# Optimization experiments

Measured on AMD Instinct MI355X. Metric: run time of the kernel, lower is better.

Reference implementation:

```python
import jax, jax.numpy as jnp
import numpy as np

E = 100    # n_estimators
F = 10     # max_features
D = 100    # input feature dim
N = 8192   # batch
LAT = 2    # latent_dim
ENC_DIMS = [F, F // 2, F // 4, LAT]          # 10 -> 5 -> 2 -> 2
DEC_DIMS = [LAT, D // 4, D // 2, D]          # 2 -> 25 -> 50 -> 100


def _make_mlp(key, dims):
    ws, bs = [], []
    for i, (din, dout) in enumerate(zip(dims[:-1], dims[1:])):
        k = jax.random.fold_in(key, i)
        ws.append(jax.random.normal(k, (E, din, dout), dtype=jnp.float32) * 0.05)
        bs.append(jnp.zeros((E, dout), dtype=jnp.float32))
    return ws, bs


def setup_inputs() -> dict:
    key = jax.random.key(0)
    k_in, k_idx, k_enc, k_hi, k_lo = jax.random.split(key, 5)
    inputs = jax.random.normal(k_in, (N, D), dtype=jnp.float32)
    # per-estimator random feature subsets (original uses choice w/o replacement)
    randsamples = jax.random.randint(k_idx, (E, F), 0, D, dtype=jnp.int32)
    enc_ws, enc_bs = _make_mlp(k_enc, ENC_DIMS)
    hi_ws, hi_bs = _make_mlp(k_hi, DEC_DIMS)
    lo_ws, lo_bs = _make_mlp(k_lo, DEC_DIMS)
    d = {"inputs": inputs, "randsamples": randsamples}
    for i in range(3):
        d[f"enc_w{i}"], d[f"enc_b{i}"] = enc_ws[i], enc_bs[i]
        d[f"hi_w{i}"], d[f"hi_b{i}"] = hi_ws[i], hi_bs[i]
        d[f"lo_w{i}"], d[f"lo_b{i}"] = lo_ws[i], lo_bs[i]
    return d


def _mlp(x, ws, bs):
    # x: [E, N, din]; linear activation throughout (module default)
    for w, b in zip(ws, bs):
        x = jnp.einsum('enf,efg->eng', x, w) + b[:, None, :]
    return x


def reference(inputs, randsamples,
              enc_w0, enc_b0, enc_w1, enc_b1, enc_w2, enc_b2,
              hi_w0, hi_b0, hi_w1, hi_b1, hi_w2, hi_b2,
              lo_w0, lo_b0, lo_w1, lo_b1, lo_w2, lo_b2):
    # batched feature gather: [N, E, F] -> [E, N, F]
    xg = jnp.transpose(jnp.take(inputs, randsamples, axis=1), (1, 0, 2))
    z = _mlp(xg, [enc_w0, enc_w1, enc_w2], [enc_b0, enc_b1, enc_b2])   # [E, N, LAT]
    o_hi = _mlp(z, [hi_w0, hi_w1, hi_w2], [hi_b0, hi_b1, hi_b2])       # [E, N, D]
    o_lo = _mlp(z, [lo_w0, lo_w1, lo_w2], [lo_b0, lo_b1, lo_b2])       # [E, N, D]
    return (o_hi, o_lo)
```

## Files before the change

kernel.cpp:

```cpp
#include <hip/hip_runtime.h>

#define E_  100
#define F_  10
#define D_  100
#define N_  8192
#define TN  256
#define NTILES (N_ / TN)

typedef float f32x4 __attribute__((ext_vector_type(4)));

#define OFF_WHI  0
#define OFF_BHI  200
#define OFF_WLO  300
#define OFF_BLO  500
#define OFF_WENC 600
#define OFF_BENC 620
#define WS_PER_E 624
#define OFF_T    (E_ * WS_PER_E)
#define WS_NEED_BYTES ((size_t)(OFF_T + D_ * N_) * 4)

template <bool DO_TRANSPOSE>
__global__ __launch_bounds__(128) void prep_kernel(
    const float* __restrict__ inputs,
    const float* __restrict__ enc_w0, const float* __restrict__ enc_b0,
    const float* __restrict__ enc_w1, const float* __restrict__ enc_b1,
    const float* __restrict__ enc_w2, const float* __restrict__ enc_b2,
    const float* __restrict__ hi_w0,  const float* __restrict__ hi_b0,
    const float* __restrict__ hi_w1,  const float* __restrict__ hi_b1,
    const float* __restrict__ hi_w2,  const float* __restrict__ hi_b2,
    const float* __restrict__ lo_w0,  const float* __restrict__ lo_b0,
    const float* __restrict__ lo_w1,  const float* __restrict__ lo_b1,
    const float* __restrict__ lo_w2,  const float* __restrict__ lo_b2,
    float* __restrict__ ws)
{
    const int t = threadIdx.x;

    if (DO_TRANSPOSE && blockIdx.x >= E_) {
        const int bi = blockIdx.x - E_;
        const int n0 = (bi >> 2) * 128;
        const int d0 = (bi & 3) * 25;
        float* T = ws + OFF_T;
        const float* rowp = inputs + (size_t)(n0 + t) * D_ + d0;
#pragma unroll 5
        for (int j = 0; j < 25; ++j)
            T[(size_t)(d0 + j) * N_ + n0 + t] = rowp[j];
        return;
    }

    const int e = blockIdx.x;
    float* wsE = ws + (size_t)e * WS_PER_E;

    {
        const float* w0 = enc_w0 + e * 50;
        const float* w1 = enc_w1 + e * 10;
        const float* w2 = enc_w2 + e * 4;
        const float* b0 = enc_b0 + e * 5;
        const float* b1 = enc_b1 + e * 2;
        const float* b2 = enc_b2 + e * 2;

        __shared__ float sW01[20];
        __shared__ float sB01[2];
        if (t < 20) {
            int f = t >> 1, g = t & 1;
            float s = 0.f;
            for (int k = 0; k < 5; ++k) s += w0[f * 5 + k] * w1[k * 2 + g];
            sW01[t] = s;
        }
        if (t < 2) {
            float s = b1[t];
            for (int k = 0; k < 5; ++k) s += b0[k] * w1[k * 2 + t];
            sB01[t] = s;
        }
        __syncthreads();
        if (t < 20) {
            int f = t >> 1, g2 = t & 1;
            wsE[OFF_WENC + t] = sW01[f * 2 + 0] * w2[0 * 2 + g2]
                              + sW01[f * 2 + 1] * w2[1 * 2 + g2];
        }
        if (t < 2) {
            wsE[OFF_BENC + t] = sB01[0] * w2[0 * 2 + t] + sB01[1] * w2[1 * 2 + t] + b2[t];
        }
        __syncthreads();
    }

    __shared__ float sT[100];
    __shared__ float sU[50];
    for (int dec = 0; dec < 2; ++dec) {
        const float* w0 = (dec ? lo_w0 : hi_w0) + e * 50;
        const float* w1 = (dec ? lo_w1 : hi_w1) + e * 1250;
        const float* w2 = (dec ? lo_w2 : hi_w2) + e * 5000;
        const float* b0 = (dec ? lo_b0 : hi_b0) + e * 25;
        const float* b1 = (dec ? lo_b1 : hi_b1) + e * 50;
        const float* b2 = (dec ? lo_b2 : hi_b2) + e * 100;
        float* W = wsE + (dec ? OFF_WLO : OFF_WHI);
        float* B = wsE + (dec ? OFF_BLO : OFF_BHI);

        for (int i = t; i < 100; i += blockDim.x) {
            int a = i / 50, c = i % 50;
            float s = 0.f;
            for (int b = 0; b < 25; ++b) s += w0[a * 25 + b] * w1[b * 50 + c];
            sT[i] = s;
        }
        for (int i = t; i < 50; i += blockDim.x) {
            float s = b1[i];
            for (int b = 0; b < 25; ++b) s += b0[b] * w1[b * 50 + i];
            sU[i] = s;
        }
        __syncthreads();
        for (int i = t; i < 200; i += blockDim.x) {
            int a = i / 100, d = i % 100;
            float s = 0.f;
            for (int c = 0; c < 50; ++c) s += sT[a * 50 + c] * w2[c * 100 + d];
            W[i] = s;
        }
        for (int i = t; i < 100; i += blockDim.x) {
            float s = b2[i];
            for (int c = 0; c < 50; ++c) s += sU[c] * w2[c * 100 + i];
            B[i] = s;
        }
        __syncthreads();
    }
}

template <bool USE_T>
__global__ __launch_bounds__(256) void rancoders_main(
    const float* __restrict__ inputs,
    const int*   __restrict__ randsamples,
    const float* __restrict__ ws,
    float* __restrict__ out)
{
    const int e    = blockIdx.x >> 5;
    const int tile = blockIdx.x & (NTILES - 1);
    const int n0   = tile * TN;
    const int t    = threadIdx.x;

    __shared__ __align__(16) float sP[WS_PER_E];
    __shared__ int    sIdx[F_];
    __shared__ float2 sZ2[TN];

    const float* wsE = ws + (size_t)e * WS_PER_E;
    for (int i = t; i < 622; i += 256) sP[i] = wsE[i];
    if (t < F_) sIdx[t] = randsamples[e * F_ + t];
    __syncthreads();

    {
        float z0 = sP[OFF_BENC + 0];
        float z1 = sP[OFF_BENC + 1];
        if (USE_T) {
            const float* T = ws + OFF_T;
#pragma unroll
            for (int f = 0; f < F_; ++f) {
                float v = T[(size_t)sIdx[f] * N_ + n0 + t];
                z0 += v * sP[OFF_WENC + 2 * f + 0];
                z1 += v * sP[OFF_WENC + 2 * f + 1];
            }
        } else {
            const float* row = inputs + (size_t)(n0 + t) * D_;
#pragma unroll
            for (int f = 0; f < F_; ++f) {
                float v = row[sIdx[f]];
                z0 += v * sP[OFF_WENC + 2 * f + 0];
                z1 += v * sP[OFF_WENC + 2 * f + 1];
            }
        }
        sZ2[t] = make_float2(z0, z1);
    }
    __syncthreads();

    const int w    = t >> 6;
    const int l    = t & 63;
    const int h    = l >> 5;
    const int dq   = l & 31;
    const bool act = (dq < 25);
    const int d    = (act ? dq : 24) * 4;

    const f32x4 w0h = *(const f32x4*)&sP[OFF_WHI + d];
    const f32x4 w1h = *(const f32x4*)&sP[OFF_WHI + 100 + d];
    const f32x4 bh  = *(const f32x4*)&sP[OFF_BHI + d];
    const f32x4 w0l = *(const f32x4*)&sP[OFF_WLO + d];
    const f32x4 w1l = *(const f32x4*)&sP[OFF_WLO + 100 + d];
    const f32x4 bl  = *(const f32x4*)&sP[OFF_BLO + d];

    float* out_hi = out + (size_t)(e * N_ + n0) * D_;
    float* out_lo = out + (size_t)E_ * N_ * D_ + (size_t)(e * N_ + n0) * D_;

#pragma unroll 8
    for (int it = 0; it < TN / 16; ++it) {
        const int r0 = it * 16 + w * 4 + h;
        const float2 za = sZ2[r0];
        const float2 zb = sZ2[r0 + 2];

        f32x4 oha = za.x * w0h + za.y * w1h + bh;
        f32x4 ohb = zb.x * w0h + zb.y * w1h + bh;
        f32x4 ola = za.x * w0l + za.y * w1l + bl;
        f32x4 olb = zb.x * w0l + zb.y * w1l + bl;

        if (act) {
            const size_t off = (size_t)r0 * D_ + (size_t)d;
            *(f32x4*)&out_hi[off]            = oha;
            *(f32x4*)&out_hi[off + 2 * D_]   = ohb;
            *(f32x4*)&out_lo[off]            = ola;
            *(f32x4*)&out_lo[off + 2 * D_]   = olb;
        }
    }
}

extern "C" void kernel_launch(void* const* d_in, const int* in_sizes, int n_in,
                              void* d_out, int out_size, void* d_ws, size_t ws_size,
                              hipStream_t stream) {
    const float* inputs      = (const float*)d_in[0];
    const int*   randsamples = (const int*)d_in[1];
    const float* enc_w0 = (const float*)d_in[2];
    const float* enc_b0 = (const float*)d_in[3];
    const float* hi_w0  = (const float*)d_in[4];
    const float* hi_b0  = (const float*)d_in[5];
    const float* lo_w0  = (const float*)d_in[6];
    const float* lo_b0  = (const float*)d_in[7];
    const float* enc_w1 = (const float*)d_in[8];
    const float* enc_b1 = (const float*)d_in[9];
    const float* hi_w1  = (const float*)d_in[10];
    const float* hi_b1  = (const float*)d_in[11];
    const float* lo_w1  = (const float*)d_in[12];
    const float* lo_b1  = (const float*)d_in[13];
    const float* enc_w2 = (const float*)d_in[14];
    const float* enc_b2 = (const float*)d_in[15];
    const float* hi_w2  = (const float*)d_in[16];
    const float* hi_b2  = (const float*)d_in[17];
    const float* lo_w2  = (const float*)d_in[18];
    const float* lo_b2  = (const float*)d_in[19];

    float* ws  = (float*)d_ws;
    float* out = (float*)d_out;

    const bool use_t = (ws_size >= WS_NEED_BYTES);

    if (use_t) {
        prep_kernel<true><<<E_ + 256, 128, 0, stream>>>(
            inputs,
            enc_w0, enc_b0, enc_w1, enc_b1, enc_w2, enc_b2,
            hi_w0, hi_b0, hi_w1, hi_b1, hi_w2, hi_b2,
            lo_w0, lo_b0, lo_w1, lo_b1, lo_w2, lo_b2, ws);
        rancoders_main<true><<<E_ * NTILES, 256, 0, stream>>>(
            inputs, randsamples, ws, out);
    } else {
        prep_kernel<false><<<E_, 128, 0, stream>>>(
            inputs,
            enc_w0, enc_b0, enc_w1, enc_b1, enc_w2, enc_b2,
            hi_w0, hi_b0, hi_w1, hi_b1, hi_w2, hi_b2,
            lo_w0, lo_b0, lo_w1, lo_b1, lo_w2, lo_b2, ws);
        rancoders_main<false><<<E_ * NTILES, 256, 0, stream>>>(
            inputs, randsamples, ws, out);
    }
}
```

Measured before the change: 150.5 us.

## Split main kernel into latent-compute pass and per-decoder store pass

When workspace allows, the latent z computation moves into its own kernel that writes z to a global buffer. A separate store kernel then launches twice as many blocks, one decoder half each, to write outputs. The aim is more parallelism and smaller per-block work for the output-bandwidth-bound store phase. The cost is an extra launch plus a z buffer write and read, and the path only runs if the workspace is large enough.

```diff
diff --git a/kernel.cpp b/kernel.cpp
--- a/kernel.cpp
+++ b/kernel.cpp
@@ -9,15 +9,10 @@
 
 typedef float f32x4 __attribute__((ext_vector_type(4)));
 
-#define OFF_WHI  0
-#define OFF_BHI  200
-#define OFF_WLO  300
-#define OFF_BLO  500
-#define OFF_WENC 600
-#define OFF_BENC 620
 #define WS_PER_E 624
-#define OFF_T    (E_ * WS_PER_E)
-#define WS_NEED_BYTES ((size_t)(OFF_T + D_ * N_) * 4)
+#define CMB_FLOATS (E_ * WS_PER_E)
+#define Z_FLOATS   (2 * E_ * N_)
+#define T_FLOATS   (D_ * N_)
 
 template <bool DO_TRANSPOSE>
 __global__ __launch_bounds__(128) void prep_kernel(
@@ -31,7 +26,7 @@
     const float* __restrict__ lo_w0,  const float* __restrict__ lo_b0,
     const float* __restrict__ lo_w1,  const float* __restrict__ lo_b1,
     const float* __restrict__ lo_w2,  const float* __restrict__ lo_b2,
-    float* __restrict__ ws)
+    float* __restrict__ cmb, float* __restrict__ T)
 {
     const int t = threadIdx.x;
 
@@ -39,7 +34,6 @@
         const int bi = blockIdx.x - E_;
         const int n0 = (bi >> 2) * 128;
         const int d0 = (bi & 3) * 25;
-        float* T = ws + OFF_T;
         const float* rowp = inputs + (size_t)(n0 + t) * D_ + d0;
 #pragma unroll 5
         for (int j = 0; j < 25; ++j)
@@ -48,7 +42,7 @@
     }
 
     const int e = blockIdx.x;
-    float* wsE = ws + (size_t)e * WS_PER_E;
+    float* wsE = cmb + (size_t)e * WS_PER_E;
 
     {
         const float* w0 = enc_w0 + e * 50;
@@ -74,11 +68,11 @@
         __syncthreads();
         if (t < 20) {
             int f = t >> 1, g2 = t & 1;
-            wsE[OFF_WENC + t] = sW01[f * 2 + 0] * w2[0 * 2 + g2]
-                              + sW01[f * 2 + 1] * w2[1 * 2 + g2];
+            wsE[600 + t] = sW01[f * 2 + 0] * w2[0 * 2 + g2]
+                         + sW01[f * 2 + 1] * w2[1 * 2 + g2];
         }
         if (t < 2) {
-            wsE[OFF_BENC + t] = sB01[0] * w2[0 * 2 + t] + sB01[1] * w2[1 * 2 + t] + b2[t];
+            wsE[620 + t] = sB01[0] * w2[0 * 2 + t] + sB01[1] * w2[1 * 2 + t] + b2[t];
         }
         __syncthreads();
     }
@@ -92,8 +86,8 @@
         const float* b0 = (dec ? lo_b0 : hi_b0) + e * 25;
         const float* b1 = (dec ? lo_b1 : hi_b1) + e * 50;
         const float* b2 = (dec ? lo_b2 : hi_b2) + e * 100;
-        float* W = wsE + (dec ? OFF_WLO : OFF_WHI);
-        float* B = wsE + (dec ? OFF_BLO : OFF_BHI);
+        float* W = wsE + (dec ? 300 : 0);
+        float* B = wsE + (dec ? 500 : 200);
 
         for (int i = t; i < 100; i += blockDim.x) {
             int a = i / 50, c = i % 50;
@@ -122,11 +116,89 @@
     }
 }
 
+__global__ __launch_bounds__(256) void z_kernel(
+    const float* __restrict__ cmb, const int* __restrict__ randsamples,
+    const float* __restrict__ T, float2* __restrict__ zbuf)
+{
+    const int e    = blockIdx.x >> 5;
+    const int tile = blockIdx.x & (NTILES - 1);
+    const int n0   = tile * TN;
+    const int t    = threadIdx.x;
+
+    __shared__ float sW[22];
+    __shared__ int   sIdx[F_];
+    if (t < 22) sW[t] = cmb[(size_t)e * WS_PER_E + 600 + t];
+    if (t < F_) sIdx[t] = randsamples[e * F_ + t];
+    __syncthreads();
+
+    float z0 = sW[20];
+    float z1 = sW[21];
+#pragma unroll
+    for (int f = 0; f < F_; ++f) {
+        const float v = T[(size_t)sIdx[f] * N_ + n0 + t];
+        z0 += v * sW[2 * f + 0];
+        z1 += v * sW[2 * f + 1];
+    }
+    zbuf[(size_t)e * N_ + n0 + t] = make_float2(z0, z1);
+}
+
+__global__ __launch_bounds__(256) void rancoders_store(
+    const float* __restrict__ cmb, const float2* __restrict__ zbuf,
+    float* __restrict__ out)
+{
+    const int b    = blockIdx.x;
+    const int half = (b >= E_ * NTILES) ? 1 : 0;
+    const int rem  = b - half * E_ * NTILES;
+    const int e    = rem >> 5;
+    const int tile = rem & (NTILES - 1);
+    const int n0   = tile * TN;
+    const int t    = threadIdx.x;
+
+    __shared__ __align__(16) float  sW[304];
+    __shared__ float2 sZ[TN];
+
+    {
+        const float* src = cmb + (size_t)e * WS_PER_E + (half ? 300 : 0);
+        for (int i = t; i < 300; i += 256) sW[i] = src[i];
+        const float2* zsrc = zbuf + (size_t)e * N_ + n0;
+        sZ[t] = zsrc[t];
+    }
+    __syncthreads();
+
+    const int w    = t >> 6;
+    const int l    = t & 63;
+    const int h    = l >> 5;
+    const int dq   = l & 31;
+    const bool act = (dq < 25);
+    const int d    = (act ? dq : 24) * 4;
+
+    const f32x4 w0 = *(const f32x4*)&sW[0 + d];
+    const f32x4 w1 = *(const f32x4*)&sW[100 + d];
+    const f32x4 bb = *(const f32x4*)&sW[200 + d];
+
+    float* dst = out + (size_t)half * E_ * N_ * D_ + (size_t)(e * N_ + n0) * D_;
+
+#pragma unroll 8
+    for (int it = 0; it < TN / 16; ++it) {
+        const int r0 = it * 16 + w * 4 + h;
+        const float2 za = sZ[r0];
+        const float2 zb = sZ[r0 + 2];
+
+        f32x4 oa = za.x * w0 + za.y * w1 + bb;
+        f32x4 ob = zb.x * w0 + zb.y * w1 + bb;
+
+        if (act) {
+            const size_t off = (size_t)r0 * D_ + (size_t)d;
+            *(f32x4*)&dst[off]          = oa;
+            *(f32x4*)&dst[off + 2 * D_] = ob;
+        }
+    }
+}
+
 template <bool USE_T>
-__global__ __launch_bounds__(256) void rancoders_main(
-    const float* __restrict__ inputs,
-    const int*   __restrict__ randsamples,
-    const float* __restrict__ ws,
+__global__ __launch_bounds__(256) void rancoders_mono(
+    const float* __restrict__ inputs, const int* __restrict__ randsamples,
+    const float* __restrict__ cmb, const float* __restrict__ T,
     float* __restrict__ out)
 {
     const int e    = blockIdx.x >> 5;
@@ -138,29 +210,27 @@
     __shared__ int    sIdx[F_];
     __shared__ float2 sZ2[TN];
 
-    const float* wsE = ws + (size_t)e * WS_PER_E;
+    const float* wsE = cmb + (size_t)e * WS_PER_E;
     for (int i = t; i < 622; i += 256) sP[i] = wsE[i];
     if (t < F_) sIdx[t] = randsamples[e * F_ + t];
     __syncthreads();
 
     {
-        float z0 = sP[OFF_BENC + 0];
-        float z1 = sP[OFF_BENC + 1];
+        float z0 = sP[620], z1 = sP[621];
         if (USE_T) {
-            const float* T = ws + OFF_T;
 #pragma unroll
             for (int f = 0; f < F_; ++f) {
                 float v = T[(size_t)sIdx[f] * N_ + n0 + t];
-                z0 += v * sP[OFF_WENC + 2 * f + 0];
-                z1 += v * sP[OFF_WENC + 2 * f + 1];
+                z0 += v * sP[600 + 2 * f + 0];
+                z1 += v * sP[600 + 2 * f + 1];
             }
         } else {
             const float* row = inputs + (size_t)(n0 + t) * D_;
 #pragma unroll
             for (int f = 0; f < F_; ++f) {
                 float v = row[sIdx[f]];
-                z0 += v * sP[OFF_WENC + 2 * f + 0];
-                z1 += v * sP[OFF_WENC + 2 * f + 1];
+                z0 += v * sP[600 + 2 * f + 0];
+                z1 += v * sP[600 + 2 * f + 1];
             }
         }
         sZ2[t] = make_float2(z0, z1);
@@ -174,12 +244,12 @@
     const bool act = (dq < 25);
     const int d    = (act ? dq : 24) * 4;
 
-    const f32x4 w0h = *(const f32x4*)&sP[OFF_WHI + d];
-    const f32x4 w1h = *(const f32x4*)&sP[OFF_WHI + 100 + d];
-    const f32x4 bh  = *(const f32x4*)&sP[OFF_BHI + d];
-    const f32x4 w0l = *(const f32x4*)&sP[OFF_WLO + d];
-    const f32x4 w1l = *(const f32x4*)&sP[OFF_WLO + 100 + d];
-    const f32x4 bl  = *(const f32x4*)&sP[OFF_BLO + d];
+    const f32x4 w0h = *(const f32x4*)&sP[0 + d];
+    const f32x4 w1h = *(const f32x4*)&sP[100 + d];
+    const f32x4 bh  = *(const f32x4*)&sP[200 + d];
+    const f32x4 w0l = *(const f32x4*)&sP[300 + d];
+    const f32x4 w1l = *(const f32x4*)&sP[400 + d];
+    const f32x4 bl  = *(const f32x4*)&sP[500 + d];
 
     float* out_hi = out + (size_t)(e * N_ + n0) * D_;
     float* out_lo = out + (size_t)E_ * N_ * D_ + (size_t)(e * N_ + n0) * D_;
@@ -189,18 +259,16 @@
         const int r0 = it * 16 + w * 4 + h;
         const float2 za = sZ2[r0];
         const float2 zb = sZ2[r0 + 2];
-
         f32x4 oha = za.x * w0h + za.y * w1h + bh;
         f32x4 ohb = zb.x * w0h + zb.y * w1h + bh;
         f32x4 ola = za.x * w0l + za.y * w1l + bl;
         f32x4 olb = zb.x * w0l + zb.y * w1l + bl;
-
         if (act) {
             const size_t off = (size_t)r0 * D_ + (size_t)d;
-            *(f32x4*)&out_hi[off]            = oha;
-            *(f32x4*)&out_hi[off + 2 * D_]   = ohb;
-            *(f32x4*)&out_lo[off]            = ola;
-            *(f32x4*)&out_lo[off + 2 * D_]   = olb;
+            *(f32x4*)&out_hi[off]          = oha;
+            *(f32x4*)&out_hi[off + 2 * D_] = ohb;
+            *(f32x4*)&out_lo[off]          = ola;
+            *(f32x4*)&out_lo[off + 2 * D_] = olb;
         }
     }
 }
@@ -232,23 +300,36 @@
     float* ws  = (float*)d_ws;
     float* out = (float*)d_out;
 
-    const bool use_t = (ws_size >= WS_NEED_BYTES);
-
-    if (use_t) {
+    const size_t need_full = (size_t)(CMB_FLOATS + Z_FLOATS + T_FLOATS) * 4;
+    const size_t need_t    = (size_t)(CMB_FLOATS + T_FLOATS) * 4;
+
+    float* cmb = ws;
+
+    if (ws_size >= need_full) {
+        float*  zbuf = ws + CMB_FLOATS;
+        float*  T    = ws + CMB_FLOATS + Z_FLOATS;
         prep_kernel<true><<<E_ + 256, 128, 0, stream>>>(
-            inputs,
-            enc_w0, enc_b0, enc_w1, enc_b1, enc_w2, enc_b2,
+            inputs, enc_w0, enc_b0, enc_w1, enc_b1, enc_w2, enc_b2,
             hi_w0, hi_b0, hi_w1, hi_b1, hi_w2, hi_b2,
-            lo_w0, lo_b0, lo_w1, lo_b1, lo_w2, lo_b2, ws);
-        rancoders_main<true><<<E_ * NTILES, 256, 0, stream>>>(
-            inputs, randsamples, ws, out);
+            lo_w0, lo_b0, lo_w1, lo_b1, lo_w2, lo_b2, cmb, T);
+        z_kernel<<<E_ * NTILES, 256, 0, stream>>>(
+            cmb, randsamples, T, (float2*)zbuf);
+        rancoders_store<<<2 * E_ * NTILES, 256, 0, stream>>>(
+            cmb, (const float2*)zbuf, out);
+    } else if (ws_size >= need_t) {
+        float* T = ws + CMB_FLOATS;
+        prep_kernel<true><<<E_ + 256, 128, 0, stream>>>(
+            inputs, enc_w0, enc_b0, enc_w1, enc_b1, enc_w2, enc_b2,
+            hi_w0, hi_b0, hi_w1, hi_b1, hi_w2, hi_b2,
+            lo_w0, lo_b0, lo_w1, lo_b1, lo_w2, lo_b2, cmb, T);
+        rancoders_mono<true><<<E_ * NTILES, 256, 0, stream>>>(
+            inputs, randsamples, cmb, T, out);
     } else {
         prep_kernel<false><<<E_, 128, 0, stream>>>(
-            inputs,
-            enc_w0, enc_b0, enc_w1, enc_b1, enc_w2, enc_b2,
+            inputs, enc_w0, enc_b0, enc_w1, enc_b1, enc_w2, enc_b2,
             hi_w0, hi_b0, hi_w1, hi_b1, hi_w2, hi_b2,
-            lo_w0, lo_b0, lo_w1, lo_b1, lo_w2, lo_b2, ws);
-        rancoders_main<false><<<E_ * NTILES, 256, 0, stream>>>(
-            inputs, randsamples, ws, out);
-    }
-}
+            lo_w0, lo_b0, lo_w1, lo_b1, lo_w2, lo_b2, cmb, nullptr);
+        rancoders_mono<false><<<E_ * NTILES, 256, 0, stream>>>(
+            inputs, randsamples, cmb, nullptr, out);
+    }
+}
```

Result: slower. 155.3 us (+3.2%).
